# Performance work log

Hardware: AMD Instinct MI355X
Metric: run time of the kernel (lower is better)

Reference implementation:

```python
import jax, jax.numpy as jnp
import numpy as np

# PointPillars scatter: B batches, C pillar-feature channels, HxW BEV grid, P pillars total.
B, C, H, W, P = 4, 64, 512, 512, 409600


def setup_inputs() -> dict:
    key = jax.random.key(0)
    k1, k2, k3 = jax.random.split(key, 3)
    voxel_features = jax.random.normal(k1, (P, C), dtype=jnp.float32)
    # coords columns: [batch_idx, z, y, x]; batch idx covers 0..B-1 so batch_size = B.
    bidx = jnp.arange(P, dtype=jnp.int32) % B
    ys = jax.random.randint(k2, (P,), 0, H, dtype=jnp.int32)
    xs = jax.random.randint(k3, (P,), 0, W, dtype=jnp.int32)
    coords = jnp.stack([bidx, jnp.zeros((P,), jnp.int32), ys, xs], axis=1)
    return {"voxel_features": voxel_features, "coords": coords}


def reference(voxel_features, coords):
    # Single-pass scatter replacing the nested python loops: compute a flat BEV
    # out-of-range pillars dropped, matching the bounds check in the loop).
    b = coords[:, 0].astype(jnp.int32)
    y = coords[:, 2].astype(jnp.int32)
    x = coords[:, 3].astype(jnp.int32)
    valid = (y >= 0) & (y < H) & (x >= 0) & (x < W)
    flat = (b * H + y) * W + x  # [P]
    flat = jnp.where(valid, flat, B * H * W)  # route invalid to OOB -> dropped
    canvas = jnp.zeros((B * H * W, C), voxel_features.dtype)
    canvas = canvas.at[flat].set(voxel_features, mode="drop")
    # [B*H*W, C] -> [B, C, H, W]
    return canvas.reshape(B, H, W, C).transpose(0, 3, 1, 2)
```

## Files before the change

### kernel.cpp

```cpp
#include <hip/hip_runtime.h>

#define BB 4
#define CC 64
#define HH 512
#define WW 512
#define PP 409600

typedef float vfloat4 __attribute__((ext_vector_type(4)));
typedef int   vint4   __attribute__((ext_vector_type(4)));

__global__ void pillar_winner_kernel(const vint4* __restrict__ coords,
                                     int* __restrict__ winner) {
    int p = blockIdx.x * blockDim.x + threadIdx.x;
    if (p >= PP) return;
    vint4 c = __builtin_nontemporal_load(coords + p);
    int b = c.x, y = c.z, x = c.w;
    if ((unsigned)y < (unsigned)HH && (unsigned)x < (unsigned)WW &&
        (unsigned)b < (unsigned)BB) {
        int flat = (b * HH + y) * WW + x;
        atomicMax(&winner[flat], p);
    }
}

__global__ void canvas_write_kernel(const float* __restrict__ feat,
                                    const int* __restrict__ winner,
                                    float* __restrict__ out) {
    int idx = blockIdx.x * blockDim.x + threadIdx.x;
    int x4   = idx & (WW / 4 - 1);
    int rest = idx >> 7;
    int y    = rest & (HH - 1);
    int b    = rest >> 9;

    int cell = (b * HH + y) * WW + x4 * 4;
    vint4 w = __builtin_nontemporal_load((const vint4*)(winner + cell));

    const vfloat4 zero = (vfloat4)(0.f);
    const vfloat4* fq = (const vfloat4*)feat;

    int obase = ((b * CC) * HH + y) * WW + x4 * 4;

#pragma unroll
    for (int c4 = 0; c4 < CC / 4; ++c4) {
        vfloat4 a  = (w.x >= 0) ? fq[w.x * (CC / 4) + c4] : zero;
        vfloat4 bq = (w.y >= 0) ? fq[w.y * (CC / 4) + c4] : zero;
        vfloat4 cq = (w.z >= 0) ? fq[w.z * (CC / 4) + c4] : zero;
        vfloat4 dq = (w.w >= 0) ? fq[w.w * (CC / 4) + c4] : zero;

        vfloat4 o0 = {a.x, bq.x, cq.x, dq.x};
        vfloat4 o1 = {a.y, bq.y, cq.y, dq.y};
        vfloat4 o2 = {a.z, bq.z, cq.z, dq.z};
        vfloat4 o3 = {a.w, bq.w, cq.w, dq.w};

        int base = obase + (c4 * 4) * (HH * WW);
        __builtin_nontemporal_store(o0, (vfloat4*)(out + base));
        __builtin_nontemporal_store(o1, (vfloat4*)(out + base + 1 * HH * WW));
        __builtin_nontemporal_store(o2, (vfloat4*)(out + base + 2 * HH * WW));
        __builtin_nontemporal_store(o3, (vfloat4*)(out + base + 3 * HH * WW));
    }
}

extern "C" void kernel_launch(void* const* d_in, const int* in_sizes, int n_in,
                              void* d_out, int out_size, void* d_ws, size_t ws_size,
                              hipStream_t stream) {
    const float* feat   = (const float*)d_in[0];
    const vint4* coords = (const vint4*)d_in[1];
    float* out          = (float*)d_out;
    int* winner         = (int*)d_ws;

    (void)hipMemsetAsync(winner, 0xFF, (size_t)BB * HH * WW * sizeof(int), stream);

    {
        int threads = 256;
        int blocks = (PP + threads - 1) / threads;
        pillar_winner_kernel<<<blocks, threads, 0, stream>>>(coords, winner);
    }

    {
        int threads = 256;
        int total = BB * HH * WW / 4;
        int blocks = total / threads;
        canvas_write_kernel<<<blocks, threads, 0, stream>>>(feat, winner, out);
    }
}
```

Before: 417.5 us.

## Transpose canvas tiles through shared memory for coalesced gather and store

Each block now covers a 128-cell row tile. It gathers the winner pillars' feature vectors with coalesced 16-byte loads, transposes them through padded LDS, and writes contiguous 512-byte channel rows to the NCHW output. The old scheme had each thread gather four scattered feature rows and write strided outputs. The change also drops the nontemporal hints on the coords load and output stores and adds launch bounds. In exchange it adds about 33KB of LDS per block, two barriers, and LDS bank traffic.

```diff
diff --git a/kernel.cpp b/kernel.cpp
--- a/kernel.cpp
+++ b/kernel.cpp
@@ -6,6 +6,9 @@
 #define WW 512
 #define PP 409600
 
+#define TILE 128
+#define SMS  129
+
 typedef float vfloat4 __attribute__((ext_vector_type(4)));
 typedef int   vint4   __attribute__((ext_vector_type(4)));
 
@@ -13,7 +16,7 @@
                                      int* __restrict__ winner) {
     int p = blockIdx.x * blockDim.x + threadIdx.x;
     if (p >= PP) return;
-    vint4 c = __builtin_nontemporal_load(coords + p);
+    vint4 c = coords[p];
     int b = c.x, y = c.z, x = c.w;
     if ((unsigned)y < (unsigned)HH && (unsigned)x < (unsigned)WW &&
         (unsigned)b < (unsigned)BB) {
@@ -22,40 +25,55 @@
     }
 }
 
+__launch_bounds__(256, 4)
 __global__ void canvas_write_kernel(const float* __restrict__ feat,
                                     const int* __restrict__ winner,
                                     float* __restrict__ out) {
-    int idx = blockIdx.x * blockDim.x + threadIdx.x;
-    int x4   = idx & (WW / 4 - 1);
-    int rest = idx >> 7;
+    __shared__ float smem[CC * SMS];
+    __shared__ int   swin[TILE];
+
+    int blk  = blockIdx.x;
+    int tx   = blk & (WW / TILE - 1);
+    int rest = blk >> 2;
     int y    = rest & (HH - 1);
     int b    = rest >> 9;
 
-    int cell = (b * HH + y) * WW + x4 * 4;
-    vint4 w = __builtin_nontemporal_load((const vint4*)(winner + cell));
+    int tid = threadIdx.x;
+    int cellbase = (b * HH + y) * WW + tx * TILE;
 
+    if (tid < TILE) swin[tid] = winner[cellbase + tid];
+    __syncthreads();
+
+    const vfloat4* fq  = (const vfloat4*)feat;
     const vfloat4 zero = (vfloat4)(0.f);
-    const vfloat4* fq = (const vfloat4*)feat;
-
-    int obase = ((b * CC) * HH + y) * WW + x4 * 4;
 
 #pragma unroll
-    for (int c4 = 0; c4 < CC / 4; ++c4) {
-        vfloat4 a  = (w.x >= 0) ? fq[w.x * (CC / 4) + c4] : zero;
-        vfloat4 bq = (w.y >= 0) ? fq[w.y * (CC / 4) + c4] : zero;
-        vfloat4 cq = (w.z >= 0) ? fq[w.z * (CC / 4) + c4] : zero;
-        vfloat4 dq = (w.w >= 0) ? fq[w.w * (CC / 4) + c4] : zero;
+    for (int i = 0; i < 8; ++i) {
+        int flat = i * 256 + tid;
+        int r = flat >> 4;
+        int k = flat & 15;
+        int w = swin[r];
+        vfloat4 v = (w >= 0) ? fq[w * (CC / 4) + k] : zero;
+        int c0 = 4 * k;
+        smem[(c0 + 0) * SMS + r] = v.x;
+        smem[(c0 + 1) * SMS + r] = v.y;
+        smem[(c0 + 2) * SMS + r] = v.z;
+        smem[(c0 + 3) * SMS + r] = v.w;
+    }
+    __syncthreads();
 
-        vfloat4 o0 = {a.x, bq.x, cq.x, dq.x};
-        vfloat4 o1 = {a.y, bq.y, cq.y, dq.y};
-        vfloat4 o2 = {a.z, bq.z, cq.z, dq.z};
-        vfloat4 o3 = {a.w, bq.w, cq.w, dq.w};
-
-        int base = obase + (c4 * 4) * (HH * WW);
-        __builtin_nontemporal_store(o0, (vfloat4*)(out + base));
-        __builtin_nontemporal_store(o1, (vfloat4*)(out + base + 1 * HH * WW));
-        __builtin_nontemporal_store(o2, (vfloat4*)(out + base + 2 * HH * WW));
-        __builtin_nontemporal_store(o3, (vfloat4*)(out + base + 3 * HH * WW));
+#pragma unroll
+    for (int i = 0; i < 8; ++i) {
+        int flat = i * 256 + tid;
+        int c  = flat >> 5;
+        int xg = flat & 31;
+        vfloat4 o;
+        o.x = smem[c * SMS + 4 * xg + 0];
+        o.y = smem[c * SMS + 4 * xg + 1];
+        o.z = smem[c * SMS + 4 * xg + 2];
+        o.w = smem[c * SMS + 4 * xg + 3];
+        int addr = ((b * CC + c) * HH + y) * WW + tx * TILE + 4 * xg;
+        *(vfloat4*)(out + addr) = o;
     }
 }
 
@@ -77,8 +95,7 @@
 
     {
         int threads = 256;
-        int total = BB * HH * WW / 4;
-        int blocks = total / threads;
+        int blocks = BB * HH * (WW / TILE);
         canvas_write_kernel<<<blocks, threads, 0, stream>>>(feat, winner, out);
     }
 }
```

Measured after the change: 383.7 us. -8.1%, faster.
